# Kernel optimization log

Measured on AMD Instinct MI355X. Metric: run time of the kernel, lower is better.

The kernel has to match this reference:

```python
import jax, jax.numpy as jnp
import numpy as np

BS = 64          # batch size (bs = x.shape[0] / prev_num_nodes)
N_COARSE = 2562  # prev_num_nodes (refinement level r)
N_FINE = 10242   # num_nodes (refinement level r+1)
E_FINE = 61440   # directed edges per sample (~6 per mesh vertex)
C_IN, C_OUT = 128, 64


def setup_inputs() -> dict:
    key = jax.random.key(0)
    k1, k2, k3 = jax.random.split(key, 3)
    x = jax.random.normal(k1, (BS * N_COARSE, C_IN), jnp.float32)
    # xavier-uniform-like init per reset_parameters (scale immaterial for correctness)
    W = jax.random.normal(k2, (C_IN, C_OUT), jnp.float32) * (1.0 / np.sqrt(C_IN))
    b = jnp.zeros((C_OUT,), jnp.float32)  # bias init to 0 per reset_parameters
    # per-sample random fine-graph edges, block-shifted like check_bs does
    e = jax.random.randint(k3, (2, BS, E_FINE), 0, N_FINE)
    shifts = jnp.arange(BS, dtype=e.dtype) * N_FINE
    edge_index = (e + shifts[None, :, None]).reshape(2, BS * E_FINE)
    # coarse vertices are the first N_COARSE fine vertices of each block
    unpool_mask = (jnp.arange(N_COARSE, dtype=jnp.int64)[None, :]
                   + (jnp.arange(BS, dtype=jnp.int64) * N_FINE)[:, None]).reshape(-1)
    return {"x": x, "W": W, "b": b, "edge_index": edge_index,
            "unpool_mask": unpool_mask}


def reference(x, W, b, edge_index, unpool_mask):
    N = BS * N_FINE  # total fine nodes (static, = max(edge_index)+1 in original)
    # --- unpooler: scatter coarse features into fine node positions ---
    up = jnp.zeros((N, x.shape[1]), x.dtype).at[unpool_mask].set(x)
    # --- GCN convolution with self-loops and symmetric normalization ---
    h = up @ W  # [N, C_OUT]
    src, dst = edge_index[0], edge_index[1]
    ones = jnp.ones(src.shape, h.dtype)
    deg = jax.ops.segment_sum(ones, dst, num_segments=N) + 1.0  # +1 self-loop
    norm = jax.lax.rsqrt(deg)  # [N]
    coef = (norm[src] * norm[dst])[:, None]          # edge normalization
    agg = jax.ops.segment_sum(h[src] * coef, dst, num_segments=N)
    agg = agg + h * (norm * norm)[:, None]           # self-loop contribution
    # --- ELU activation ---
    return jax.nn.elu(agg + b)
```

## Files before the change

kernel.cpp:

```cpp
#include <hip/hip_runtime.h>
#include <hip/hip_bf16.h>
#include <math.h>

#define CIN 128
#define COUT 64
#define BSAMP 64
#define NFINE 10242
#define NCOARSE 2562
#define NRNG 4
#define RS 2561
#define HT 1024
#define NCLS 17
#define SEGCAP 20480
#define CPAD 16

typedef float f32x4 __attribute__((ext_vector_type(4)));
typedef short s16x8 __attribute__((ext_vector_type(8)));

__global__ __launch_bounds__(256) void k_zero(int* __restrict__ cur, int n) {
    int i = blockIdx.x * 256 + threadIdx.x;
    if (i < n) cur[i] = 0;
}

__global__ __launch_bounds__(256) void k_prep(const int4* __restrict__ src4, const int4* __restrict__ dst4,
                                              unsigned* __restrict__ pk, int* __restrict__ cur,
                                              int EPS, int bps) {
    __shared__ unsigned bbuf[NRNG][1024];
    __shared__ int bcnt[NRNG];
    __shared__ int gb[NRNG];
    int t = threadIdx.x;
    int b  = blockIdx.x / bps;
    int il = (blockIdx.x % bps) * 256 + t;
    int n4 = EPS / 4;
    if (t < NRNG) bcnt[t] = 0;
    __syncthreads();
    if (il < n4) {
        size_t i = (size_t)b * n4 + il;
        int4 s = src4[i], d = dst4[i];
        int base = b * NFINE;
#define COMP(c) { \
        int ls = d.c - base; \
        if ((unsigned)ls < (unsigned)NFINE) { \
            int rri = ls / RS; \
            int sl = s.c - base; \
            unsigned rc = ((unsigned)sl < (unsigned)NCOARSE) ? (unsigned)(b * NCOARSE + sl + 1) : 0u; \
            unsigned pv = ((unsigned)(ls - rri * RS) << 18) | rc; \
            int p = atomicAdd(&bcnt[rri], 1); \
            bbuf[rri][p] = pv; } }
        COMP(x) COMP(y) COMP(z) COMP(w)
#undef COMP
    }
    __syncthreads();
    if (t < NRNG) gb[t] = atomicAdd(&cur[(b * NRNG + t) * CPAD], bcnt[t]);
    __syncthreads();
#pragma unroll
    for (int rr = 0; rr < NRNG; ++rr) {
        int n = bcnt[rr];
        int g0 = gb[rr];
        unsigned* seg = pk + (size_t)(b * NRNG + rr) * SEGCAP;
        for (int i = t; i < n; i += 256) {
            int pos = g0 + i;
            if (pos < SEGCAP) seg[pos] = bbuf[rr][i];
        }
    }
}

__global__ __launch_bounds__(HT) void k_build(const unsigned* __restrict__ pk, const int* __restrict__ cur,
                                              int2* __restrict__ meta, float* __restrict__ normc,
                                              int* __restrict__ vals, int* __restrict__ ord,
                                              int* __restrict__ gctr) {
    __shared__ int   lh[RS];
    __shared__ int   sm[HT];
    __shared__ int   ccnt[NCLS];
    __shared__ int   gbase;
    int t = threadIdx.x;
    int b = blockIdx.x / NRNG, r = blockIdx.x % NRNG;
    int lo = r * RS;
    int nlocal = min(RS, NFINE - lo);
    int rebase = b * NFINE + lo;
    for (int j = t; j < nlocal; j += HT) lh[j] = 0;
    if (t < NCLS) ccnt[t] = 0;
    __syncthreads();

    const unsigned* seg = pk + (size_t)(b * NRNG + r) * SEGCAP;
    int ne = min(cur[(b * NRNG + r) * CPAD], SEGCAP);
    for (int i = t; i < ne; i += HT) {
        unsigned u = seg[i];
        int l = (int)(u >> 18);
        int rc = (int)(u & 0x3FFFFu);
        if (l < nlocal) atomicAdd(&lh[l], 1 + (rc ? 65536 : 0));
    }
    __syncthreads();

    int mj[3], degk[3], selfk[3], cls[3], rank[3];
    int psum = 0;
#pragma unroll
    for (int k = 0; k < 3; ++k) {
        int idx = t + k * HT;
        int m = 0, dg = 0, sf = 0;
        if (idx < nlocal) {
            int c = lh[idx];
            int slocal = lo + idx;
            sf = (slocal < NCOARSE) ? (b * NCOARSE + slocal + 1) : 0;
            m = (c >> 16) + (sf ? 1 : 0);
            dg = (c & 0xFFFF) + 1;
            cls[k] = min(m, NCLS - 1);
            rank[k] = atomicAdd(&ccnt[cls[k]], 1);
        }
        mj[k] = m; degk[k] = dg; selfk[k] = sf;
        psum += m;
    }
    sm[t] = psum; __syncthreads();
    for (int off = 1; off < HT; off <<= 1) {
        int add = (t >= off) ? sm[t - off] : 0;
        __syncthreads();
        sm[t] += add;
        __syncthreads();
    }
    if (t == HT - 1) gbase = atomicAdd(gctr, sm[HT - 1]);
    if (t == 0) {
        int run = 0;
#pragma unroll
        for (int c = 0; c < NCLS; ++c) { int v = ccnt[c]; ccnt[c] = run; run += v; }
    }
    __syncthreads();

    int run = gbase + sm[t] - psum;
#pragma unroll
    for (int k = 0; k < 3; ++k) {
        int idx = t + k * HT;
        if (idx < nlocal) {
            int gf = rebase + idx;
            meta[gf] = make_int2(run, mj[k] | (degk[k] << 16));
            ord[rebase + ccnt[cls[k]] + rank[k]] = gf;
            int cur2 = run;
            if (selfk[k]) {
                int rv = selfk[k] - 1;
                normc[rv] = rsqrtf((float)degk[k]);
                vals[cur2] = rv;
                ++cur2;
            }
            lh[idx] = cur2;
            run += mj[k];
        }
    }
    __syncthreads();

    for (int i = t; i < ne; i += HT) {
        unsigned u = seg[i];
        int l = (int)(u >> 18);
        int rc = (int)(u & 0x3FFFFu);
        if (rc && l < nlocal) {
            int pos = atomicAdd(&lh[l], 1);
            vals[pos] = rc - 1;
        }
    }
}

__global__ __launch_bounds__(256) void k_gemm(const float* __restrict__ x, const float* __restrict__ W,
                                              const float* __restrict__ normc,
                                              __hip_bfloat16* __restrict__ h, int M) {
    __shared__ unsigned short sWT[COUT][CIN + 8];
    int t = threadIdx.x;
    for (int i = t; i < CIN * COUT; i += 256) {
        int k = i >> 6, c = i & 63;
        __hip_bfloat16 v = __float2bfloat16(W[i]);
        sWT[c][k] = *reinterpret_cast<unsigned short*>(&v);
    }
    __syncthreads();

    int wid  = t >> 6;
    int lane = t & 63;
    int r0 = blockIdx.x * 64 + wid * 16;
    if (r0 >= M) return;
    int row = lane & 15;
    int kg  = lane >> 4;

    s16x8 bf[4][4];
#pragma unroll
    for (int ct = 0; ct < 4; ++ct)
#pragma unroll
        for (int ks = 0; ks < 4; ++ks)
            bf[ct][ks] = *reinterpret_cast<const s16x8*>(&sWT[ct * 16 + row][ks * 32 + kg * 8]);

    const float* xr = x + (size_t)(r0 + row) * CIN + kg * 8;
    s16x8 af[4];
#pragma unroll
    for (int ks = 0; ks < 4; ++ks) {
        float4 a0 = *reinterpret_cast<const float4*>(xr + ks * 32);
        float4 a1 = *reinterpret_cast<const float4*>(xr + ks * 32 + 4);
        alignas(16) __hip_bfloat16 tmp[8];
        tmp[0] = __float2bfloat16(a0.x); tmp[1] = __float2bfloat16(a0.y);
        tmp[2] = __float2bfloat16(a0.z); tmp[3] = __float2bfloat16(a0.w);
        tmp[4] = __float2bfloat16(a1.x); tmp[5] = __float2bfloat16(a1.y);
        tmp[6] = __float2bfloat16(a1.z); tmp[7] = __float2bfloat16(a1.w);
        af[ks] = *reinterpret_cast<const s16x8*>(tmp);
    }

    f32x4 acc[4] = { (f32x4)(0.f), (f32x4)(0.f), (f32x4)(0.f), (f32x4)(0.f) };
#pragma unroll
    for (int ks = 0; ks < 4; ++ks)
#pragma unroll
        for (int ct = 0; ct < 4; ++ct)
            acc[ct] = __builtin_amdgcn_mfma_f32_16x16x32_bf16(af[ks], bf[ct][ks], acc[ct], 0, 0, 0);

    float sc[4];
#pragma unroll
    for (int j = 0; j < 4; ++j) sc[j] = normc[r0 + kg * 4 + j];
#pragma unroll
    for (int ct = 0; ct < 4; ++ct) {
#pragma unroll
        for (int j = 0; j < 4; ++j) {
            int rr = r0 + kg * 4 + j;
            h[(size_t)rr * COUT + ct * 16 + row] = __float2bfloat16(acc[ct][j] * sc[j]);
        }
    }
}

__global__ __launch_bounds__(256) void k_gather(const __hip_bfloat16* __restrict__ h, const int2* __restrict__ meta,
                                                const int* __restrict__ vals, const int* __restrict__ ord,
                                                const float* __restrict__ b, float* __restrict__ out, int N32) {
    int wid  = (blockIdx.x * 256 + threadIdx.x) >> 6;
    int lane = threadIdx.x & 63;
    if (wid >= N32) return;
    int g  = lane >> 4;
    int il = lane & 15;
    int base = wid * 32;
    f32x4 bb = *reinterpret_cast<const f32x4*>(&b[il * 4]);

    int nid[8], bg[8], mm[8], mx[8];
    float nf[8];
    f32x4 acc[8];
    int mmax = 0;
#pragma unroll
    for (int s = 0; s < 8; ++s) {
        nid[s] = ord[base + 4 * s + g];
        int2 Mi = meta[nid[s]];
        bg[s] = Mi.x;
        mm[s] = Mi.y & 0xFFFF;
        nf[s] = rsqrtf((float)(Mi.y >> 16));
        int m1 = max(mm[s], __shfl_xor(mm[s], 16));
        mx[s] = max(m1, __shfl_xor(m1, 32));
        acc[s] = (f32x4)(0.f);
        mmax = max(mmax, mx[s]);
    }
    const char* hb = (const char*)h;
    for (int j = 0; j < mmax; ++j) {
#pragma unroll
        for (int s = 0; s < 8; ++s) {
            if (j < mx[s]) {
                bool act = j < mm[s];
                int e = act ? vals[bg[s] + j] : 0;
                uint2 hw = act ? *(const uint2*)(hb + (((size_t)(unsigned)e) << 7) + il * 8)
                               : make_uint2(0u, 0u);
                acc[s].x += __uint_as_float(hw.x << 16);
                acc[s].y += __uint_as_float(hw.x & 0xFFFF0000u);
                acc[s].z += __uint_as_float(hw.y << 16);
                acc[s].w += __uint_as_float(hw.y & 0xFFFF0000u);
            }
        }
    }
#pragma unroll
    for (int s = 0; s < 8; ++s) {
        f32x4 v;
        v.x = fmaf(acc[s].x, nf[s], bb.x);
        v.y = fmaf(acc[s].y, nf[s], bb.y);
        v.z = fmaf(acc[s].z, nf[s], bb.z);
        v.w = fmaf(acc[s].w, nf[s], bb.w);
        v.x = v.x > 0.f ? v.x : (__expf(v.x) - 1.0f);
        v.y = v.y > 0.f ? v.y : (__expf(v.y) - 1.0f);
        v.z = v.z > 0.f ? v.z : (__expf(v.z) - 1.0f);
        v.w = v.w > 0.f ? v.w : (__expf(v.w) - 1.0f);
        f32x4* dstp = (f32x4*)(out + ((size_t)(unsigned)nid[s]) * COUT + il * 4);
        __builtin_nontemporal_store(v, dstp);
    }
}

extern "C" void kernel_launch(void* const* d_in, const int* in_sizes, int n_in,
                              void* d_out, int out_size, void* d_ws, size_t ws_size,
                              hipStream_t stream) {
    const float* x    = (const float*)d_in[0];
    const float* W    = (const float*)d_in[1];
    const float* b    = (const float*)d_in[2];
    const int*   edge = (const int*)d_in[3];
    const int Mx = in_sizes[0] / CIN;
    const int E  = in_sizes[3] / 2;
    const int N  = out_size / COUT;
    const int EPS = E / BSAMP;

    const int* src = edge;
    const int* dst = edge + E;

    char* ws = (char*)d_ws;
    int2*  meta   = (int2*)ws;     ws += (size_t)N * 8;
    int*   cur    = (int*)ws;      ws += (256 * CPAD + 256) * 4;
    float* normc  = (float*)ws;    ws += (size_t)Mx * 4;
    int*   ord    = (int*)ws;      ws += (size_t)N * 4;
    __hip_bfloat16* h = (__hip_bfloat16*)ws;
    unsigned* pk  = (unsigned*)ws;
    {
        size_t hbytes  = (size_t)Mx * COUT * 2;
        size_t pkbytes = (size_t)BSAMP * NRNG * SEGCAP * 4;
        ws += (hbytes > pkbytes ? hbytes : pkbytes);
    }
    int*   vals   = (int*)ws;

    int* gctr = cur + 256 * CPAD;
    const int bps = (EPS / 4 + 255) / 256;
    const int nzero = 256 * CPAD + 1;

    k_zero  <<<(nzero + 255) / 256, 256, 0, stream>>>(cur, nzero);
    k_prep  <<<BSAMP * bps, 256, 0, stream>>>((const int4*)src, (const int4*)dst, pk, cur, EPS, bps);
    k_build <<<BSAMP * NRNG, HT, 0, stream>>>(pk, cur, meta, normc, vals, ord, gctr);
    k_gemm  <<<(Mx + 63) / 64, 256, 0, stream>>>(x, W, normc, h, Mx);
    k_gather<<<((N / 32) * 64 + 255) / 256, 256, 0, stream>>>(h, meta, vals, ord, b, (float*)d_out, N / 32);
}
```

Measured before the change: 149.8 us.

## Aggregate LDS atomics per wave, nontemporal x loads, swizzle gather blocks, memset

In the edge-bucketing kernel, per-lane LDS atomicAdd on the range counters is replaced by a wave-level ballot that has one leader per range do a single atomic, with slots assigned by popcount. The GEMM loads x with nontemporal hints to avoid polluting cache, and the gather kernel remaps block IDs in groups of 8, likely aiming at better spread across XCDs and L2 locality. The zeroing kernel is replaced by hipMemsetAsync. Together these trim LDS contention and launch overhead, at the cost of extra ballot and shuffle work per range in the prep kernel.

```diff
diff --git a/kernel.cpp b/kernel.cpp
--- a/kernel.cpp
+++ b/kernel.cpp
@@ -17,11 +17,6 @@
 typedef float f32x4 __attribute__((ext_vector_type(4)));
 typedef short s16x8 __attribute__((ext_vector_type(8)));
 
-__global__ __launch_bounds__(256) void k_zero(int* __restrict__ cur, int n) {
-    int i = blockIdx.x * 256 + threadIdx.x;
-    if (i < n) cur[i] = 0;
-}
-
 __global__ __launch_bounds__(256) void k_prep(const int4* __restrict__ src4, const int4* __restrict__ dst4,
                                               unsigned* __restrict__ pk, int* __restrict__ cur,
                                               int EPS, int bps) {
@@ -32,24 +27,34 @@
     int b  = blockIdx.x / bps;
     int il = (blockIdx.x % bps) * 256 + t;
     int n4 = EPS / 4;
+    int lane = t & 63;
+    unsigned long long lmask = (1ull << lane) - 1ull;
     if (t < NRNG) bcnt[t] = 0;
     __syncthreads();
-    if (il < n4) {
-        size_t i = (size_t)b * n4 + il;
-        int4 s = src4[i], d = dst4[i];
-        int base = b * NFINE;
+    bool valid = il < n4;
+    size_t i = (size_t)b * n4 + (valid ? il : 0);
+    int4 s = src4[i], d = dst4[i];
+    int base = b * NFINE;
 #define COMP(c) { \
-        int ls = d.c - base; \
-        if ((unsigned)ls < (unsigned)NFINE) { \
-            int rri = ls / RS; \
-            int sl = s.c - base; \
-            unsigned rc = ((unsigned)sl < (unsigned)NCOARSE) ? (unsigned)(b * NCOARSE + sl + 1) : 0u; \
-            unsigned pv = ((unsigned)(ls - rri * RS) << 18) | rc; \
-            int p = atomicAdd(&bcnt[rri], 1); \
-            bbuf[rri][p] = pv; } }
-        COMP(x) COMP(y) COMP(z) COMP(w)
+    int ls = d.c - base; \
+    bool ve = valid && ((unsigned)ls < (unsigned)NFINE); \
+    int rri = ve ? (ls / RS) : -1; \
+    int sl = s.c - base; \
+    unsigned rc = ((unsigned)sl < (unsigned)NCOARSE) ? (unsigned)(b * NCOARSE + sl + 1) : 0u; \
+    unsigned pv = ve ? ((((unsigned)(ls - rri * RS)) << 18) | rc) : 0u; \
+    _Pragma("unroll") \
+    for (int rr = 0; rr < NRNG; ++rr) { \
+        unsigned long long m = __ballot(ve && (rri == rr)); \
+        if (m) { \
+            int leader = __ffsll((unsigned long long)m) - 1; \
+            int wb = 0; \
+            if (lane == leader) wb = atomicAdd(&bcnt[rr], __popcll(m)); \
+            wb = __shfl(wb, leader); \
+            if (ve && rri == rr) bbuf[rr][wb + (int)__popcll(m & lmask)] = pv; \
+        } \
+    } }
+    COMP(x) COMP(y) COMP(z) COMP(w)
 #undef COMP
-    }
     __syncthreads();
     if (t < NRNG) gb[t] = atomicAdd(&cur[(b * NRNG + t) * CPAD], bcnt[t]);
     __syncthreads();
@@ -58,9 +63,9 @@
         int n = bcnt[rr];
         int g0 = gb[rr];
         unsigned* seg = pk + (size_t)(b * NRNG + rr) * SEGCAP;
-        for (int i = t; i < n; i += 256) {
-            int pos = g0 + i;
-            if (pos < SEGCAP) seg[pos] = bbuf[rr][i];
+        for (int i2 = t; i2 < n; i2 += 256) {
+            int pos = g0 + i2;
+            if (pos < SEGCAP) seg[pos] = bbuf[rr][i2];
         }
     }
 }
@@ -187,8 +192,8 @@
     s16x8 af[4];
 #pragma unroll
     for (int ks = 0; ks < 4; ++ks) {
-        float4 a0 = *reinterpret_cast<const float4*>(xr + ks * 32);
-        float4 a1 = *reinterpret_cast<const float4*>(xr + ks * 32 + 4);
+        f32x4 a0 = __builtin_nontemporal_load(reinterpret_cast<const f32x4*>(xr + ks * 32));
+        f32x4 a1 = __builtin_nontemporal_load(reinterpret_cast<const f32x4*>(xr + ks * 32 + 4));
         alignas(16) __hip_bfloat16 tmp[8];
         tmp[0] = __float2bfloat16(a0.x); tmp[1] = __float2bfloat16(a0.y);
         tmp[2] = __float2bfloat16(a0.z); tmp[3] = __float2bfloat16(a0.w);
@@ -220,7 +225,10 @@
 __global__ __launch_bounds__(256) void k_gather(const __hip_bfloat16* __restrict__ h, const int2* __restrict__ meta,
                                                 const int* __restrict__ vals, const int* __restrict__ ord,
                                                 const float* __restrict__ b, float* __restrict__ out, int N32) {
-    int wid  = (blockIdx.x * 256 + threadIdx.x) >> 6;
+    int nblk = gridDim.x;
+    int bid = blockIdx.x;
+    if ((nblk & 7) == 0) { int c = nblk >> 3; bid = (bid & 7) * c + (bid >> 3); }
+    int wid  = (bid * 256 + (int)threadIdx.x) >> 6;
     int lane = threadIdx.x & 63;
     if (wid >= N32) return;
     int g  = lane >> 4;
@@ -305,13 +313,12 @@
     }
     int*   vals   = (int*)ws;
 
-    int* gctr = cur + 256 * CPAD;
     const int bps = (EPS / 4 + 255) / 256;
     const int nzero = 256 * CPAD + 1;
 
-    k_zero  <<<(nzero + 255) / 256, 256, 0, stream>>>(cur, nzero);
+    hipMemsetAsync(cur, 0, (size_t)nzero * 4, stream);
     k_prep  <<<BSAMP * bps, 256, 0, stream>>>((const int4*)src, (const int4*)dst, pk, cur, EPS, bps);
-    k_build <<<BSAMP * NRNG, HT, 0, stream>>>(pk, cur, meta, normc, vals, ord, gctr);
+    k_build <<<BSAMP * NRNG, HT, 0, stream>>>(pk, cur, meta, normc, vals, ord, cur + 256 * CPAD);
     k_gemm  <<<(Mx + 63) / 64, 256, 0, stream>>>(x, W, normc, h, Mx);
     k_gather<<<((N / 32) * 64 + 255) / 256, 256, 0, stream>>>(h, meta, vals, ord, b, (float*)d_out, N / 32);
 }
```

After: 162.7 us. +8.6%, slower.
